# Performance work log

Hardware: AMD Instinct MI355X
Metric: run time of the kernel (lower is better)

Reference implementation:

```python
import jax, jax.numpy as jnp
import numpy as np

EPS = 1e-6

def setup_inputs() -> dict:
    key = jax.random.key(0)
    k1, k2, k3, k4, k5 = jax.random.split(key, 5)
    B, Lq, Lk, D, Dc = 8, 1024, 8192, 256, 128
    q = jax.random.normal(k1, (B, Lq, D), dtype=jnp.float32)
    k_q = jax.random.randint(k2, (B, Lk, Dc), 0, 16, dtype=jnp.int32)  # 4-bit codes
    k_scale = jax.random.uniform(k3, (B, 1, Dc), dtype=jnp.float32)
    k_zero = jax.random.uniform(k4, (B, 1, Dc), dtype=jnp.float32) * 15.0
    W_up = jax.random.normal(k5, (D, Dc), dtype=jnp.float32) / np.sqrt(Dc)
    return {"q": q, "k_q": k_q, "k_scale": k_scale, "k_zero": k_zero, "W_up": W_up}

def reference(q, k_q, k_scale, k_zero, W_up):
    # int4 dequantization: (B, Lk, Dc)
    k_c = k_scale * (k_q.astype(jnp.float32) - k_zero)
    # low-rank decompress (nn.Linear(d_compressed, d_model, bias=False)): k = k_c @ W_up.T -> (B, Lk, D)
    k = jnp.einsum('blc,dc->bld', k_c, W_up)
    # squared norms (raw values used in diff, clamped values used in denominator)
    q_sq = jnp.sum(q * q, axis=-1)  # (B, Lq)
    k_sq = jnp.sum(k * k, axis=-1)  # (B, Lk)
    q_norm_sq = jnp.minimum(q_sq, 1.0 - EPS)
    k_norm_sq = jnp.minimum(k_sq, 1.0 - EPS)
    # ||q_i - k_j||^2 via expansion (same math as materializing the diff tensor)
    qk = jnp.einsum('bqd,bkd->bqk', q, k)  # (B, Lq, Lk)
    diff_norm_sq = jnp.maximum(q_sq[:, :, None] + k_sq[:, None, :] - 2.0 * qk, 0.0)
    denom = (1.0 - q_norm_sq)[:, :, None] * (1.0 - k_norm_sq)[:, None, :] + EPS
    dist = jnp.arccosh(1.0 + 2.0 * diff_norm_sq / denom)  # (B, Lq, Lk)
    return dist
```

## Files before the change

### kernel.cpp

```cpp
#include <hip/hip_runtime.h>
#include <hip/hip_bf16.h>

#define B_   8
#define LQ   1024
#define LK   8192
#define D_   256
#define DC   128
#define EPSF 1e-6f

typedef __attribute__((ext_vector_type(8))) short short8;
typedef __attribute__((ext_vector_type(4))) float floatx4;

static __device__ __forceinline__ floatx4 mfma16(short8 a, short8 b, floatx4 c) {
    return __builtin_amdgcn_mfma_f32_16x16x32_bf16(a, b, c, 0, 0, 0);
}
static __device__ __forceinline__ float fast_rcp(float x)  { return __builtin_amdgcn_rcpf(x); }
static __device__ __forceinline__ float fast_sqrt(float x) { return __builtin_amdgcn_sqrtf(x); }
static __device__ __forceinline__ float fast_ln(float x)   { return 0.69314718056f * __builtin_amdgcn_logf(x); }

__global__ __launch_bounds__(256) void k_G(const float* __restrict__ W,
                                           __hip_bfloat16* __restrict__ G) {
    __shared__ float red[128];
    int c1 = blockIdx.x;
    int t = threadIdx.x, c2 = t & 127, h = t >> 7;
    int d0 = h * 128;
    float a0 = 0.f, a1 = 0.f, a2 = 0.f, a3 = 0.f;
#pragma unroll 4
    for (int d = 0; d < 128; d += 4) {
        a0 += W[(size_t)(d0 + d + 0) * DC + c1] * W[(size_t)(d0 + d + 0) * DC + c2];
        a1 += W[(size_t)(d0 + d + 1) * DC + c1] * W[(size_t)(d0 + d + 1) * DC + c2];
        a2 += W[(size_t)(d0 + d + 2) * DC + c1] * W[(size_t)(d0 + d + 2) * DC + c2];
        a3 += W[(size_t)(d0 + d + 3) * DC + c1] * W[(size_t)(d0 + d + 3) * DC + c2];
    }
    float s = (a0 + a1) + (a2 + a3);
    if (h) red[c2] = s;
    __syncthreads();
    if (!h) G[c1 * DC + c2] = __float2bfloat16(s + red[c2]);
}

__global__ __launch_bounds__(256) void k_qproj(const float* __restrict__ q,
                                               const float* __restrict__ W,
                                               __hip_bfloat16* __restrict__ qproj,
                                               float* __restrict__ q_sq) {
    __shared__ __hip_bfloat16 sA[64 * 72];
    __shared__ __hip_bfloat16 sB[128 * 72];
    int t = threadIdx.x, lane = t & 63, w = t >> 6;
    int quad = lane >> 4, li = lane & 15;
    int row0 = blockIdx.x * 64;

    float psum[4] = {0.f, 0.f, 0.f, 0.f};
    floatx4 acc[8];
#pragma unroll
    for (int nt = 0; nt < 8; ++nt) acc[nt] = (floatx4){0.f, 0.f, 0.f, 0.f};

    for (int kc4 = 0; kc4 < 4; ++kc4) {
#pragma unroll
        for (int it = 0; it < 4; ++it) {
            int idx = it * 256 + t;
            int r = idx >> 4, pos = idx & 15;
            float4 v = *(const float4*)(q + (size_t)(row0 + r) * D_ + kc4 * 64 + pos * 4);
            psum[it] += v.x * v.x + v.y * v.y + v.z * v.z + v.w * v.w;
            __hip_bfloat16* dst = &sA[r * 72 + pos * 4];
            dst[0] = __float2bfloat16(v.x); dst[1] = __float2bfloat16(v.y);
            dst[2] = __float2bfloat16(v.z); dst[3] = __float2bfloat16(v.w);
        }
#pragma unroll
        for (int it = 0; it < 32; ++it) {
            int e = it * 256 + t;
            int dl = e >> 7, c = e & 127;
            sB[c * 72 + dl] = __float2bfloat16(W[(size_t)(kc4 * 64 + dl) * DC + c]);
        }
        __syncthreads();
        short8 af[2];
#pragma unroll
        for (int ks = 0; ks < 2; ++ks)
            af[ks] = *(const short8*)&sA[(w * 16 + li) * 72 + ks * 32 + quad * 8];
#pragma unroll
        for (int nt = 0; nt < 8; ++nt)
#pragma unroll
            for (int ks = 0; ks < 2; ++ks) {
                short8 bf = *(const short8*)&sB[(nt * 16 + li) * 72 + ks * 32 + quad * 8];
                acc[nt] = mfma16(af[ks], bf, acc[nt]);
            }
        __syncthreads();
    }
#pragma unroll
    for (int nt = 0; nt < 8; ++nt)
#pragma unroll
        for (int r = 0; r < 4; ++r) {
            int row = w * 16 + quad * 4 + r;
            qproj[(size_t)(row0 + row) * DC + nt * 16 + li] = __float2bfloat16(acc[nt][r]);
        }
#pragma unroll
    for (int it = 0; it < 4; ++it) {
        float s = psum[it];
        s += __shfl_xor(s, 1); s += __shfl_xor(s, 2);
        s += __shfl_xor(s, 4); s += __shfl_xor(s, 8);
        if (li == 0) q_sq[row0 + it * 16 + w * 4 + quad] = s;
    }
}

__global__ __launch_bounds__(256) void k_dq_ksq(const int* __restrict__ kq,
                                                const float* __restrict__ kscale,
                                                const float* __restrict__ kzero,
                                                const __hip_bfloat16* __restrict__ G,
                                                __hip_bfloat16* __restrict__ kc,
                                                float* __restrict__ k_sq) {
    __shared__ __hip_bfloat16 sK[128 * 132];
    int t = threadIdx.x, lane = t & 63, w = t >> 6;
    int quad = lane >> 4, li = lane & 15;
    int b = blockIdx.x >> 6, l0 = (blockIdx.x & 63) * 128;

    const int4* codes = (const int4*)(kq + ((size_t)b * LK + l0) * DC);
    int col = (t & 31) * 4;
    float4 sc = *(const float4*)(kscale + b * DC + col);
    float4 zp = *(const float4*)(kzero + b * DC + col);
    __hip_bfloat16* kco = kc + ((size_t)b * LK + l0) * DC;
#pragma unroll
    for (int it = 0; it < 16; ++it) {
        int idx = it * 256 + t;
        int r = idx >> 5;
        int4 c4 = codes[idx];
        __hip_bfloat16 tmp[4];
        tmp[0] = __float2bfloat16(sc.x * ((float)c4.x - zp.x));
        tmp[1] = __float2bfloat16(sc.y * ((float)c4.y - zp.y));
        tmp[2] = __float2bfloat16(sc.z * ((float)c4.z - zp.z));
        tmp[3] = __float2bfloat16(sc.w * ((float)c4.w - zp.w));
        *(uint2*)&sK[r * 132 + col] = *(const uint2*)tmp;
        *(uint2*)(kco + idx * 4)    = *(const uint2*)tmp;
    }
    __syncthreads();

    short8 af[2][4];
#pragma unroll
    for (int mt = 0; mt < 2; ++mt)
#pragma unroll
        for (int ks = 0; ks < 4; ++ks)
            af[mt][ks] = *(const short8*)&sK[(w * 32 + mt * 16 + li) * 132 + ks * 32 + quad * 8];
    float s[2][4] = {{0, 0, 0, 0}, {0, 0, 0, 0}};
#pragma unroll
    for (int nt = 0; nt < 8; ++nt) {
        floatx4 a0 = (floatx4){0.f, 0.f, 0.f, 0.f};
        floatx4 a1 = (floatx4){0.f, 0.f, 0.f, 0.f};
#pragma unroll
        for (int ks = 0; ks < 4; ++ks) {
            short8 bf = *(const short8*)(G + (size_t)(nt * 16 + li) * DC + ks * 32 + quad * 8);
            a0 = mfma16(af[0][ks], bf, a0);
            a1 = mfma16(af[1][ks], bf, a1);
        }
        int c2 = nt * 16 + li;
#pragma unroll
        for (int r = 0; r < 4; ++r) {
            int r0 = w * 32 +      quad * 4 + r;
            int r1 = w * 32 + 16 + quad * 4 + r;
            s[0][r] += a0[r] * __bfloat162float(sK[r0 * 132 + c2]);
            s[1][r] += a1[r] * __bfloat162float(sK[r1 * 132 + c2]);
        }
    }
#pragma unroll
    for (int mt = 0; mt < 2; ++mt)
#pragma unroll
        for (int r = 0; r < 4; ++r) {
            float v = s[mt][r];
            v += __shfl_xor(v, 1); v += __shfl_xor(v, 2);
            v += __shfl_xor(v, 4); v += __shfl_xor(v, 8);
            if (li == 0)
                k_sq[(size_t)b * LK + l0 + w * 32 + mt * 16 + quad * 4 + r] = v;
        }
}

__global__ __launch_bounds__(256) void k_main(const __hip_bfloat16* __restrict__ qproj,
                                              const __hip_bfloat16* __restrict__ kc,
                                              const float* __restrict__ q_sq,
                                              const float* __restrict__ k_sq,
                                              float* __restrict__ out) {
    __shared__ __hip_bfloat16 sA[128 * 72];
    __shared__ __hip_bfloat16 sB[128 * 72];
    int t = threadIdx.x, lane = t & 63, w = t >> 6;
    int quad = lane >> 4, li = lane & 15;
    int wm = w >> 1, wn = w & 1;
    int n0 = blockIdx.x * 128, m0 = blockIdx.y * 128, b = blockIdx.z;
    const uint4* Ag = (const uint4*)(qproj + ((size_t)b * LQ + m0) * DC);
    const uint4* Bg = (const uint4*)(kc   + ((size_t)b * LK + n0) * DC);
    uint4* dA = (uint4*)sA; uint4* dB = (uint4*)sB;

    floatx4 acc[4][4];
#pragma unroll
    for (int i = 0; i < 4; ++i)
#pragma unroll
        for (int j = 0; j < 4; ++j)
            acc[i][j] = (floatx4){0.f, 0.f, 0.f, 0.f};

    int r_ = t >> 3, ch_ = t & 7;
    uint4 ra[4], rb[4];
#pragma unroll
    for (int it = 0; it < 4; ++it) {
        ra[it] = Ag[(it * 32 + r_) * 16 + ch_];
        rb[it] = Bg[(it * 32 + r_) * 16 + ch_];
    }
#pragma unroll
    for (int it = 0; it < 4; ++it) {
        dA[(it * 32 + r_) * 9 + ch_] = ra[it];
        dB[(it * 32 + r_) * 9 + ch_] = rb[it];
    }
    __syncthreads();
#pragma unroll
    for (int it = 0; it < 4; ++it) {
        ra[it] = Ag[(it * 32 + r_) * 16 + 8 + ch_];
        rb[it] = Bg[(it * 32 + r_) * 16 + 8 + ch_];
    }
#pragma unroll
    for (int ks = 0; ks < 2; ++ks) {
        short8 qf[4], kf[4];
#pragma unroll
        for (int i = 0; i < 4; ++i) {
            qf[i] = *(const short8*)&sA[(wm * 64 + i * 16 + li) * 72 + ks * 32 + quad * 8];
            kf[i] = *(const short8*)&sB[(wn * 64 + i * 16 + li) * 72 + ks * 32 + quad * 8];
        }
#pragma unroll
        for (int i = 0; i < 4; ++i)
#pragma unroll
            for (int j = 0; j < 4; ++j)
                acc[i][j] = mfma16(kf[j], qf[i], acc[i][j]);
    }
    __syncthreads();
#pragma unroll
    for (int it = 0; it < 4; ++it) {
        dA[(it * 32 + r_) * 9 + ch_] = ra[it];
        dB[(it * 32 + r_) * 9 + ch_] = rb[it];
    }
    __syncthreads();
#pragma unroll
    for (int ks = 0; ks < 2; ++ks) {
        short8 qf[4], kf[4];
#pragma unroll
        for (int i = 0; i < 4; ++i) {
            qf[i] = *(const short8*)&sA[(wm * 64 + i * 16 + li) * 72 + ks * 32 + quad * 8];
            kf[i] = *(const short8*)&sB[(wn * 64 + i * 16 + li) * 72 + ks * 32 + quad * 8];
        }
#pragma unroll
        for (int i = 0; i < 4; ++i)
#pragma unroll
            for (int j = 0; j < 4; ++j)
                acc[i][j] = mfma16(kf[j], qf[i], acc[i][j]);
    }

    floatx4 ks4[4], kn4[4];
#pragma unroll
    for (int j = 0; j < 4; ++j) {
        ks4[j] = *(const floatx4*)(k_sq + (size_t)b * LK + n0 + wn * 64 + j * 16 + quad * 4);
#pragma unroll
        for (int r = 0; r < 4; ++r)
            kn4[j][r] = 1.f - fminf(ks4[j][r], 1.f - EPSF);
    }
#pragma unroll
    for (int i = 0; i < 4; ++i) {
        int m = m0 + wm * 64 + i * 16 + li;
        float qs  = q_sq[(size_t)b * LQ + m];
        float omq = 1.f - fminf(qs, 1.f - EPSF);
        float* orow = out + ((size_t)b * LQ + m) * (size_t)LK + n0 + wn * 64;
#pragma unroll
        for (int j = 0; j < 4; ++j) {
            floatx4 o;
#pragma unroll
            for (int r = 0; r < 4; ++r) {
                float diff  = fmaxf(qs + ks4[j][r] - 2.f * acc[i][j][r], 0.f);
                float delta = 2.f * diff * fast_rcp(omq * kn4[j][r] + EPSF);
                float sq    = fast_sqrt(delta * (delta + 2.f));
                o[r] = fast_ln(1.f + delta + sq);
            }
            __builtin_nontemporal_store(o, (floatx4*)(orow + j * 16 + quad * 4));
        }
    }
}

extern "C" void kernel_launch(void* const* d_in, const int* in_sizes, int n_in,
                              void* d_out, int out_size, void* d_ws, size_t ws_size,
                              hipStream_t stream) {
    const float* q      = (const float*)d_in[0];
    const int*   kq     = (const int*)d_in[1];
    const float* kscale = (const float*)d_in[2];
    const float* kzero  = (const float*)d_in[3];
    const float* W      = (const float*)d_in[4];
    float* out = (float*)d_out;

    char* ws = (char*)d_ws;
    __hip_bfloat16* qproj = (__hip_bfloat16*)(ws);
    __hip_bfloat16* kc    = (__hip_bfloat16*)(ws + 2097152);
    __hip_bfloat16* G     = (__hip_bfloat16*)(ws + 18874368);
    float*          q_sq  = (float*)(ws + 18907136);
    float*          k_sq  = (float*)(ws + 18939904);

    k_G     <<<128, 256, 0, stream>>>(W, G);
    k_qproj <<<128, 256, 0, stream>>>(q, W, qproj, q_sq);
    k_dq_ksq<<<512, 256, 0, stream>>>(kq, kscale, kzero, G, kc, k_sq);
    dim3 grid(LK / 128, LQ / 128, B_);
    k_main  <<<grid, 256, 0, stream>>>(qproj, kc, q_sq, k_sq, out);
}
```

Baseline: 384.4 us.

## Stage k_main output through LDS for coalesced rows; pre-transpose W; split dequant blocks

The k_main epilogue now writes MFMA accumulators into shared memory and reads them back so each thread stores contiguous 16-byte chunks along output rows. Before, lanes stored 16-byte pieces scattered across 16 different rows. k_G also writes a bf16 transposed copy of W, which k_qproj loads with vector uint4 reads instead of strided scalar fp32 reads. k_dq_ksq handles 64 rows per block instead of 128, doubling the grid. The price is two extra barriers and an LDS round trip in k_main, and the Wt scratch reuses the kc buffer, which is only safe because of launch ordering.

```diff
diff --git a/kernel.cpp b/kernel.cpp
--- a/kernel.cpp
+++ b/kernel.cpp
@@ -19,7 +19,8 @@
 static __device__ __forceinline__ float fast_ln(float x)   { return 0.69314718056f * __builtin_amdgcn_logf(x); }
 
 __global__ __launch_bounds__(256) void k_G(const float* __restrict__ W,
-                                           __hip_bfloat16* __restrict__ G) {
+                                           __hip_bfloat16* __restrict__ G,
+                                           __hip_bfloat16* __restrict__ Wt) {
     __shared__ float red[128];
     int c1 = blockIdx.x;
     int t = threadIdx.x, c2 = t & 127, h = t >> 7;
@@ -34,12 +35,13 @@
     }
     float s = (a0 + a1) + (a2 + a3);
     if (h) red[c2] = s;
+    Wt[(size_t)c1 * D_ + t] = __float2bfloat16(W[(size_t)t * DC + c1]);
     __syncthreads();
     if (!h) G[c1 * DC + c2] = __float2bfloat16(s + red[c2]);
 }
 
 __global__ __launch_bounds__(256) void k_qproj(const float* __restrict__ q,
-                                               const float* __restrict__ W,
+                                               const __hip_bfloat16* __restrict__ Wt,
                                                __hip_bfloat16* __restrict__ qproj,
                                                float* __restrict__ q_sq) {
     __shared__ __hip_bfloat16 sA[64 * 72];
@@ -65,10 +67,11 @@
             dst[2] = __float2bfloat16(v.z); dst[3] = __float2bfloat16(v.w);
         }
 #pragma unroll
-        for (int it = 0; it < 32; ++it) {
+        for (int it = 0; it < 4; ++it) {
             int e = it * 256 + t;
-            int dl = e >> 7, c = e & 127;
-            sB[c * 72 + dl] = __float2bfloat16(W[(size_t)(kc4 * 64 + dl) * DC + c]);
+            int c = e >> 3, ch = e & 7;
+            *(uint4*)&sB[c * 72 + ch * 8] =
+                *(const uint4*)(Wt + (size_t)c * D_ + kc4 * 64 + ch * 8);
         }
         __syncthreads();
         short8 af[2];
@@ -106,10 +109,10 @@
                                                 const __hip_bfloat16* __restrict__ G,
                                                 __hip_bfloat16* __restrict__ kc,
                                                 float* __restrict__ k_sq) {
-    __shared__ __hip_bfloat16 sK[128 * 132];
+    __shared__ __hip_bfloat16 sK[64 * 132];
     int t = threadIdx.x, lane = t & 63, w = t >> 6;
     int quad = lane >> 4, li = lane & 15;
-    int b = blockIdx.x >> 6, l0 = (blockIdx.x & 63) * 128;
+    int b = blockIdx.x >> 7, l0 = (blockIdx.x & 127) * 64;
 
     const int4* codes = (const int4*)(kq + ((size_t)b * LK + l0) * DC);
     int col = (t & 31) * 4;
@@ -117,7 +120,7 @@
     float4 zp = *(const float4*)(kzero + b * DC + col);
     __hip_bfloat16* kco = kc + ((size_t)b * LK + l0) * DC;
 #pragma unroll
-    for (int it = 0; it < 16; ++it) {
+    for (int it = 0; it < 8; ++it) {
         int idx = it * 256 + t;
         int r = idx >> 5;
         int4 c4 = codes[idx];
@@ -131,42 +134,32 @@
     }
     __syncthreads();
 
-    short8 af[2][4];
-#pragma unroll
-    for (int mt = 0; mt < 2; ++mt)
-#pragma unroll
-        for (int ks = 0; ks < 4; ++ks)
-            af[mt][ks] = *(const short8*)&sK[(w * 32 + mt * 16 + li) * 132 + ks * 32 + quad * 8];
-    float s[2][4] = {{0, 0, 0, 0}, {0, 0, 0, 0}};
+    short8 af[4];
+#pragma unroll
+    for (int ks = 0; ks < 4; ++ks)
+        af[ks] = *(const short8*)&sK[(w * 16 + li) * 132 + ks * 32 + quad * 8];
+    float s4[4] = {0.f, 0.f, 0.f, 0.f};
 #pragma unroll
     for (int nt = 0; nt < 8; ++nt) {
         floatx4 a0 = (floatx4){0.f, 0.f, 0.f, 0.f};
-        floatx4 a1 = (floatx4){0.f, 0.f, 0.f, 0.f};
 #pragma unroll
         for (int ks = 0; ks < 4; ++ks) {
             short8 bf = *(const short8*)(G + (size_t)(nt * 16 + li) * DC + ks * 32 + quad * 8);
-            a0 = mfma16(af[0][ks], bf, a0);
-            a1 = mfma16(af[1][ks], bf, a1);
+            a0 = mfma16(af[ks], bf, a0);
         }
         int c2 = nt * 16 + li;
 #pragma unroll
-        for (int r = 0; r < 4; ++r) {
-            int r0 = w * 32 +      quad * 4 + r;
-            int r1 = w * 32 + 16 + quad * 4 + r;
-            s[0][r] += a0[r] * __bfloat162float(sK[r0 * 132 + c2]);
-            s[1][r] += a1[r] * __bfloat162float(sK[r1 * 132 + c2]);
-        }
-    }
-#pragma unroll
-    for (int mt = 0; mt < 2; ++mt)
-#pragma unroll
-        for (int r = 0; r < 4; ++r) {
-            float v = s[mt][r];
-            v += __shfl_xor(v, 1); v += __shfl_xor(v, 2);
-            v += __shfl_xor(v, 4); v += __shfl_xor(v, 8);
-            if (li == 0)
-                k_sq[(size_t)b * LK + l0 + w * 32 + mt * 16 + quad * 4 + r] = v;
-        }
+        for (int r = 0; r < 4; ++r)
+            s4[r] += a0[r] * __bfloat162float(sK[(w * 16 + quad * 4 + r) * 132 + c2]);
+    }
+#pragma unroll
+    for (int r = 0; r < 4; ++r) {
+        float v = s4[r];
+        v += __shfl_xor(v, 1); v += __shfl_xor(v, 2);
+        v += __shfl_xor(v, 4); v += __shfl_xor(v, 8);
+        if (li == 0)
+            k_sq[(size_t)b * LK + l0 + w * 16 + quad * 4 + r] = v;
+    }
 }
 
 __global__ __launch_bounds__(256) void k_main(const __hip_bfloat16* __restrict__ qproj,
@@ -174,8 +167,11 @@
                                               const float* __restrict__ q_sq,
                                               const float* __restrict__ k_sq,
                                               float* __restrict__ out) {
-    __shared__ __hip_bfloat16 sA[128 * 72];
-    __shared__ __hip_bfloat16 sB[128 * 72];
+    __shared__ __align__(16) char smem[128 * 72 * 2 * 2];
+    __hip_bfloat16* sA = (__hip_bfloat16*)smem;
+    __hip_bfloat16* sB = sA + 128 * 72;
+    float* sO = (float*)smem;
+
     int t = threadIdx.x, lane = t & 63, w = t >> 6;
     int quad = lane >> 4, li = lane & 15;
     int wm = w >> 1, wn = w & 1;
@@ -245,31 +241,48 @@
                 acc[i][j] = mfma16(kf[j], qf[i], acc[i][j]);
     }
 
-    floatx4 ks4[4], kn4[4];
-#pragma unroll
-    for (int j = 0; j < 4; ++j) {
-        ks4[j] = *(const floatx4*)(k_sq + (size_t)b * LK + n0 + wn * 64 + j * 16 + quad * 4);
+    int orow_t = t >> 4;
+    int ocol4  = (t & 15) * 4;
+    float qsA[8], omqA[8];
+#pragma unroll
+    for (int qq = 0; qq < 8; ++qq) {
+        qsA[qq]  = q_sq[(size_t)b * LQ + m0 + qq * 16 + orow_t];
+        omqA[qq] = 1.f - fminf(qsA[qq], 1.f - EPSF);
+    }
+#pragma unroll
+    for (int p = 0; p < 2; ++p) {
+        __syncthreads();
+#pragma unroll
+        for (int jj = 0; jj < 2; ++jj) {
+            int c = wn * 32 + jj * 16 + quad * 4;
+#pragma unroll
+            for (int i = 0; i < 4; ++i) {
+                int m = wm * 64 + i * 16 + li;
+                *(floatx4*)&sO[m * 68 + c] = acc[i][p * 2 + jj];
+            }
+        }
+        __syncthreads();
+        int nbase = (ocol4 >> 5) * 64 + p * 32 + (ocol4 & 31);
+        floatx4 ks4 = *(const floatx4*)(k_sq + (size_t)b * LK + n0 + nbase);
+        floatx4 kn;
 #pragma unroll
         for (int r = 0; r < 4; ++r)
-            kn4[j][r] = 1.f - fminf(ks4[j][r], 1.f - EPSF);
-    }
-#pragma unroll
-    for (int i = 0; i < 4; ++i) {
-        int m = m0 + wm * 64 + i * 16 + li;
-        float qs  = q_sq[(size_t)b * LQ + m];
-        float omq = 1.f - fminf(qs, 1.f - EPSF);
-        float* orow = out + ((size_t)b * LQ + m) * (size_t)LK + n0 + wn * 64;
-#pragma unroll
-        for (int j = 0; j < 4; ++j) {
+            kn[r] = 1.f - fminf(ks4[r], 1.f - EPSF);
+#pragma unroll
+        for (int qq = 0; qq < 8; ++qq) {
+            int row = qq * 16 + orow_t;
+            floatx4 v = *(const floatx4*)&sO[row * 68 + ocol4];
+            float qs = qsA[qq], omq = omqA[qq];
             floatx4 o;
 #pragma unroll
             for (int r = 0; r < 4; ++r) {
-                float diff  = fmaxf(qs + ks4[j][r] - 2.f * acc[i][j][r], 0.f);
-                float delta = 2.f * diff * fast_rcp(omq * kn4[j][r] + EPSF);
+                float diff  = fmaxf(qs + ks4[r] - 2.f * v[r], 0.f);
+                float delta = 2.f * diff * fast_rcp(omq * kn[r] + EPSF);
                 float sq    = fast_sqrt(delta * (delta + 2.f));
                 o[r] = fast_ln(1.f + delta + sq);
             }
-            __builtin_nontemporal_store(o, (floatx4*)(orow + j * 16 + quad * 4));
+            __builtin_nontemporal_store(
+                o, (floatx4*)(out + ((size_t)b * LQ + m0 + row) * (size_t)LK + n0 + nbase));
         }
     }
 }
@@ -290,10 +303,11 @@
     __hip_bfloat16* G     = (__hip_bfloat16*)(ws + 18874368);
     float*          q_sq  = (float*)(ws + 18907136);
     float*          k_sq  = (float*)(ws + 18939904);
-
-    k_G     <<<128, 256, 0, stream>>>(W, G);
-    k_qproj <<<128, 256, 0, stream>>>(q, W, qproj, q_sq);
-    k_dq_ksq<<<512, 256, 0, stream>>>(kq, kscale, kzero, G, kc, k_sq);
+    __hip_bfloat16* Wt    = kc;
+
+    k_G     <<<128, 256, 0, stream>>>(W, G, Wt);
+    k_qproj <<<128, 256, 0, stream>>>(q, Wt, qproj, q_sq);
+    k_dq_ksq<<<1024, 256, 0, stream>>>(kq, kscale, kzero, G, kc, k_sq);
     dim3 grid(LK / 128, LQ / 128, B_);
     k_main  <<<grid, 256, 0, stream>>>(qproj, kc, q_sq, k_sq, out);
 }
```

Result: no change. 386.3 us (+0.5%).
